# Kernel optimization log

Measured on AMD Instinct MI355X. Metric: run time of the kernel, lower is better.

The kernel has to match this reference:

```python
import jax, jax.numpy as jnp
import numpy as np

N, E = 50000, 800000
IN, HID, H, OUT = 128, 32, 4, 32
NEG_SLOPE = 0.2


def _gatv2_layer(x, edge_index, Wl, bl, Wr, br, att, bias, heads, ch, concat):
    """One GATv2Conv layer (PyG semantics: add self-loops, lin_l on source,
    lin_r on target, e = att . leaky_relu(gl_src + gr_dst), segment softmax
    over incoming edges of each target, scatter-add weighted source messages)."""
    n = x.shape[0]
    loop = jnp.arange(n)
    src = jnp.concatenate([edge_index[0], loop])
    dst = jnp.concatenate([edge_index[1], loop])

    gl = (x @ Wl + bl).reshape(n, heads, ch)   # source transform [N,H,C]
    gr = (x @ Wr + br).reshape(n, heads, ch)   # target transform [N,H,C]

    m = jax.nn.leaky_relu(gl[src] + gr[dst], NEG_SLOPE)   # [E+N,H,C]
    e = jnp.einsum('ehc,hc->eh', m, att)                   # [E+N,H]

    # numerically stable segment softmax over dst
    emax = jax.lax.stop_gradient(jax.ops.segment_max(e, dst, num_segments=n))
    ex = jnp.exp(e - emax[dst])
    denom = jax.ops.segment_sum(ex, dst, num_segments=n)
    alpha = ex / denom[dst]                                # [E+N,H]

    out = jax.ops.segment_sum(alpha[:, :, None] * gl[src], dst, num_segments=n)  # [N,H,C]
    out = out.reshape(n, heads * ch) if concat else out.mean(axis=1)
    return out + bias


def setup_inputs() -> dict:
    key = jax.random.key(0)
    ks = jax.random.split(key, 16)
    s = 0.05
    return {
        'x': jax.random.normal(ks[0], (N, IN), dtype=jnp.float32),
        'edge_index': jax.random.randint(ks[1], (2, E), 0, N, dtype=jnp.int32),
        # layer 1: IN -> HID, H heads, concat
        'Wl1': jax.random.normal(ks[2], (IN, H * HID), dtype=jnp.float32) * s,
        'bl1': jnp.zeros((H * HID,), dtype=jnp.float32),
        'Wr1': jax.random.normal(ks[3], (IN, H * HID), dtype=jnp.float32) * s,
        'br1': jnp.zeros((H * HID,), dtype=jnp.float32),
        'att1': jax.random.normal(ks[4], (H, HID), dtype=jnp.float32) * s,
        'bias1': jnp.zeros((H * HID,), dtype=jnp.float32),
        # layer 2: H*HID -> OUT, 1 head, no concat
        'Wl2': jax.random.normal(ks[5], (H * HID, OUT), dtype=jnp.float32) * s,
        'bl2': jnp.zeros((OUT,), dtype=jnp.float32),
        'Wr2': jax.random.normal(ks[6], (H * HID, OUT), dtype=jnp.float32) * s,
        'br2': jnp.zeros((OUT,), dtype=jnp.float32),
        'att2': jax.random.normal(ks[7], (1, OUT), dtype=jnp.float32) * s,
        'bias2': jnp.zeros((OUT,), dtype=jnp.float32),
    }


def reference(x, edge_index, Wl1, bl1, Wr1, br1, att1, bias1,
              Wl2, bl2, Wr2, br2, att2, bias2):
    h = jax.nn.elu(_gatv2_layer(x, edge_index, Wl1, bl1, Wr1, br1, att1, bias1, H, HID, True))
    # dropout inactive in eval mode
    return _gatv2_layer(h, edge_index, Wl2, bl2, Wr2, br2, att2, bias2, 1, OUT, False)
```

## Files before the change

### kernel.cpp

```cpp
#include <hip/hip_runtime.h>

#define NNODES 50000
#define NEDGES 800000
#define ETOT   (NNODES + NEDGES)
#define NEG 0.2f
#define BKTS 196
#define P1E 4096
#define NP1 ((ETOT + P1E - 1) / P1E)

typedef unsigned short ushort_t;
typedef unsigned int uint_t;
typedef __attribute__((ext_vector_type(8))) short short8;
typedef __attribute__((ext_vector_type(4))) float f32x4;

__device__ __forceinline__ ushort_t f2bf(float f) {
  uint_t u = __float_as_uint(f);
  u += 0x7FFFu + ((u >> 16) & 1u);
  return (ushort_t)(u >> 16);
}
__device__ __forceinline__ float bf2f(ushort_t h) {
  return __uint_as_float((uint_t)h << 16);
}

__global__ __launch_bounds__(256) void coarse_hist(const int* __restrict__ ei,
                                                   int* __restrict__ pcnt) {
  __shared__ int c[BKTS];
  for (int i = threadIdx.x; i < BKTS; i += 256) c[i] = 0;
  __syncthreads();
  int e0 = blockIdx.x * P1E;
#pragma unroll
  for (int t = 0; t < P1E / 256; ++t) {
    int i = e0 + t * 256 + (int)threadIdx.x;
    if (i < ETOT) {
      int dst = (i < NEDGES) ? ei[NEDGES + i] : (i - NEDGES);
      atomicAdd(&c[dst >> 8], 1);
    }
  }
  __syncthreads();
  for (int i = threadIdx.x; i < BKTS; i += 256)
    pcnt[i * NP1 + blockIdx.x] = c[i];
}

__global__ __launch_bounds__(64) void coarse_scan(const int* __restrict__ pcnt,
                                                  int* __restrict__ goffArr,
                                                  int* __restrict__ tot) {
  int b = blockIdx.x;
  int lane = threadIdx.x;
  int carry = 0;
  for (int k0 = 0; k0 < NP1; k0 += 64) {
    int k = k0 + lane;
    int v = (k < NP1) ? pcnt[b * NP1 + k] : 0;
    int s = v;
    for (int off = 1; off < 64; off <<= 1) {
      int u = __shfl_up(s, off);
      if (lane >= off) s += u;
    }
    if (k < NP1) goffArr[b * NP1 + k] = carry + s - v;
    carry += __shfl(s, 63);
  }
  if (lane == 0) tot[b] = carry;
}

__global__ __launch_bounds__(64) void bucket_scan(const int* __restrict__ tot,
                                                  int* __restrict__ bucketStart,
                                                  int* __restrict__ rowptr) {
  int lane = threadIdx.x;
  int carry = 0;
  for (int k0 = 0; k0 < BKTS; k0 += 64) {
    int k = k0 + lane;
    int v = (k < BKTS) ? tot[k] : 0;
    int s = v;
    for (int off = 1; off < 64; off <<= 1) {
      int u = __shfl_up(s, off);
      if (lane >= off) s += u;
    }
    if (k < BKTS) bucketStart[k] = carry + s - v;
    carry += __shfl(s, 63);
  }
  if (lane == 0) {
    bucketStart[BKTS] = carry;
    rowptr[NNODES] = ETOT;
  }
}

__global__ __launch_bounds__(256) void bin_phase1(const int* __restrict__ ei,
                                                  const int* __restrict__ bucketStart,
                                                  const int* __restrict__ goffArr,
                                                  uint_t* __restrict__ binned) {
  __shared__ int cnt[BKTS], pref[BKTS], fillL[BKTS];
  __shared__ uint_t stage[P1E];
  int e0 = blockIdx.x * P1E;
  for (int i = threadIdx.x; i < BKTS; i += 256) { cnt[i] = 0; fillL[i] = 0; }
  __syncthreads();
  uint_t mypk[P1E / 256];
  int mybkt[P1E / 256];
#pragma unroll
  for (int t = 0; t < P1E / 256; ++t) {
    int i = e0 + t * 256 + (int)threadIdx.x;
    if (i < ETOT) {
      int dst = (i < NEDGES) ? ei[NEDGES + i] : (i - NEDGES);
      int src = (i < NEDGES) ? ei[i] : dst;
      int b = dst >> 8;
      mypk[t] = (uint_t)src | ((uint_t)(dst & 255) << 16) | ((uint_t)b << 24);
      mybkt[t] = b;
      atomicAdd(&cnt[b], 1);
    } else mybkt[t] = -1;
  }
  __syncthreads();
  if (threadIdx.x == 0) {
    int r = 0;
    for (int b = 0; b < BKTS; ++b) { pref[b] = r; r += cnt[b]; }
  }
  __syncthreads();
#pragma unroll
  for (int t = 0; t < P1E / 256; ++t) {
    if (mybkt[t] >= 0) {
      int p = pref[mybkt[t]] + atomicAdd(&fillL[mybkt[t]], 1);
      stage[p] = mypk[t];
    }
  }
  __syncthreads();
  int total = (e0 + P1E <= ETOT) ? P1E : (ETOT - e0);
  for (int j = threadIdx.x; j < total; j += 256) {
    uint_t pk = stage[j];
    int b = pk >> 24;
    binned[bucketStart[b] + goffArr[b * NP1 + blockIdx.x] + (j - pref[b])] = pk;
  }
}

__global__ __launch_bounds__(256) void bin_phase2(const uint_t* __restrict__ binned,
                                                  const int* __restrict__ bucketStart,
                                                  int* __restrict__ rowptr,
                                                  int* __restrict__ csrc) {
  __shared__ int cnt[256], pref[256], fillL[256];
  __shared__ int outS[8192];
  int b = blockIdx.x;
  int base = bucketStart[b];
  int cntAll = bucketStart[b + 1] - base;
  cnt[threadIdx.x] = 0; fillL[threadIdx.x] = 0;
  __syncthreads();
  for (int j = threadIdx.x; j < cntAll; j += 256)
    atomicAdd(&cnt[(binned[base + j] >> 16) & 255], 1);
  __syncthreads();
  if (threadIdx.x == 0) {
    int r = 0;
    for (int i = 0; i < 256; ++i) { pref[i] = r; r += cnt[i]; }
  }
  __syncthreads();
  int node = b * 256 + (int)threadIdx.x;
  if (node < NNODES) rowptr[node] = base + pref[threadIdx.x];
  for (int j = threadIdx.x; j < cntAll; j += 256) {
    uint_t pk = binned[base + j];
    int d = (pk >> 16) & 255;
    int p = pref[d] + atomicAdd(&fillL[d], 1);
    outS[p] = (int)(pk & 0xFFFF);
  }
  __syncthreads();
  for (int j = threadIdx.x; j < cntAll; j += 256)
    csrc[base + j] = outS[j];
}

__global__ __launch_bounds__(256) void prep_w(const float* __restrict__ Wl1,
                                              const float* __restrict__ Wr1,
                                              ushort_t* __restrict__ WtHi,
                                              ushort_t* __restrict__ WtLo) {
  int k = blockIdx.x;
  int n = threadIdx.x;
  float w = (n < 128) ? Wl1[k * 128 + n] : Wr1[k * 128 + (n - 128)];
  ushort_t h = f2bf(w);
  WtHi[n * 128 + k] = h;
  WtLo[n * 128 + k] = f2bf(w - bf2f(h));
}

__global__ __launch_bounds__(256) void gemm1_mfma(
    const float* __restrict__ x,
    const ushort_t* __restrict__ WtHi, const ushort_t* __restrict__ WtLo,
    const float* __restrict__ bl1, const float* __restrict__ br1,
    ushort_t* __restrict__ gl1, ushort_t* __restrict__ gr1) {
  constexpr int LDA = 132;
  __shared__ __align__(16) char smem[32 * 260 * 4];
  ushort_t (*Ahi)[LDA] = (ushort_t(*)[LDA])smem;
  ushort_t (*Alo)[LDA] = (ushort_t(*)[LDA])(smem + 32 * LDA * 2);
  float (*Cs)[260] = (float(*)[260])smem;
  int m0 = blockIdx.x * 32;
  int tid = threadIdx.x;
#pragma unroll
  for (int i = 0; i < 4; ++i) {
    int it = i * 256 + tid;
    int row = it >> 5, c4 = it & 31;
    int gm = m0 + row;
    float4 v = (gm < NNODES) ? *(const float4*)&x[(size_t)gm * 128 + 4 * c4]
                             : make_float4(0.f, 0.f, 0.f, 0.f);
    ushort_t h0 = f2bf(v.x), h1 = f2bf(v.y), h2 = f2bf(v.z), h3 = f2bf(v.w);
    ushort_t l0 = f2bf(v.x - bf2f(h0)), l1 = f2bf(v.y - bf2f(h1));
    ushort_t l2 = f2bf(v.z - bf2f(h2)), l3 = f2bf(v.w - bf2f(h3));
    uint2 ph, pl;
    ph.x = (uint_t)h0 | ((uint_t)h1 << 16); ph.y = (uint_t)h2 | ((uint_t)h3 << 16);
    pl.x = (uint_t)l0 | ((uint_t)l1 << 16); pl.y = (uint_t)l2 | ((uint_t)l3 << 16);
    *(uint2*)&Ahi[row][4 * c4] = ph;
    *(uint2*)&Alo[row][4 * c4] = pl;
  }
  __syncthreads();
  int wave = tid >> 6, lane = tid & 63;
  int quad = lane >> 4, nl = lane & 15;
  int nb = wave * 64;
  f32x4 acc[2][4];
#pragma unroll
  for (int tm = 0; tm < 2; ++tm)
#pragma unroll
    for (int tn = 0; tn < 4; ++tn) acc[tm][tn] = (f32x4){0.f, 0.f, 0.f, 0.f};

#pragma unroll
  for (int kc = 0; kc < 4; ++kc) {
    int klane = kc * 32 + quad * 8;
    short8 ah[2], al[2], bh[4], bl[4];
#pragma unroll
    for (int tm = 0; tm < 2; ++tm) {
      ah[tm] = *(const short8*)&Ahi[16 * tm + nl][klane];
      al[tm] = *(const short8*)&Alo[16 * tm + nl][klane];
    }
#pragma unroll
    for (int tn = 0; tn < 4; ++tn) {
      size_t wo = (size_t)(nb + 16 * tn + nl) * 128 + klane;
      bh[tn] = *(const short8*)&WtHi[wo];
      bl[tn] = *(const short8*)&WtLo[wo];
    }
#pragma unroll
    for (int tm = 0; tm < 2; ++tm)
#pragma unroll
      for (int tn = 0; tn < 4; ++tn) {
        acc[tm][tn] = __builtin_amdgcn_mfma_f32_16x16x32_bf16(ah[tm], bh[tn], acc[tm][tn], 0, 0, 0);
        acc[tm][tn] = __builtin_amdgcn_mfma_f32_16x16x32_bf16(ah[tm], bl[tn], acc[tm][tn], 0, 0, 0);
        acc[tm][tn] = __builtin_amdgcn_mfma_f32_16x16x32_bf16(al[tm], bh[tn], acc[tm][tn], 0, 0, 0);
      }
  }
  float bb[4];
#pragma unroll
  for (int tn = 0; tn < 4; ++tn) {
    int n = nb + 16 * tn + nl;
    bb[tn] = (n < 128) ? bl1[n] : br1[n - 128];
  }
  __syncthreads();
#pragma unroll
  for (int tm = 0; tm < 2; ++tm)
#pragma unroll
    for (int tn = 0; tn < 4; ++tn)
#pragma unroll
      for (int r = 0; r < 4; ++r)
        Cs[16 * tm + 4 * quad + r][nb + 16 * tn + nl] = acc[tm][tn][r] + bb[tn];
  __syncthreads();
#pragma unroll
  for (int i = 0; i < 2; ++i) {
    int it = i * 256 + tid;
    int row = it >> 4, oc = (it & 15) * 8;
    int gm = m0 + row;
    if (gm < NNODES) {
      uint4 pk;
      pk.x = (uint_t)f2bf(Cs[row][oc + 0]) | ((uint_t)f2bf(Cs[row][oc + 1]) << 16);
      pk.y = (uint_t)f2bf(Cs[row][oc + 2]) | ((uint_t)f2bf(Cs[row][oc + 3]) << 16);
      pk.z = (uint_t)f2bf(Cs[row][oc + 4]) | ((uint_t)f2bf(Cs[row][oc + 5]) << 16);
      pk.w = (uint_t)f2bf(Cs[row][oc + 6]) | ((uint_t)f2bf(Cs[row][oc + 7]) << 16);
      *(uint4*)&gl1[(size_t)gm * 128 + oc] = pk;
    }
  }
#pragma unroll
  for (int i = 0; i < 2; ++i) {
    int it = i * 256 + tid;
    int row = it >> 4, oc = (it & 15) * 8;
    int gm = m0 + row;
    if (gm < NNODES) {
      uint4 pk;
      pk.x = (uint_t)f2bf(Cs[row][128 + oc + 0]) | ((uint_t)f2bf(Cs[row][128 + oc + 1]) << 16);
      pk.y = (uint_t)f2bf(Cs[row][128 + oc + 2]) | ((uint_t)f2bf(Cs[row][128 + oc + 3]) << 16);
      pk.z = (uint_t)f2bf(Cs[row][128 + oc + 4]) | ((uint_t)f2bf(Cs[row][128 + oc + 5]) << 16);
      pk.w = (uint_t)f2bf(Cs[row][128 + oc + 6]) | ((uint_t)f2bf(Cs[row][128 + oc + 7]) << 16);
      *(uint4*)&gr1[(size_t)gm * 128 + oc] = pk;
    }
  }
}

__global__ __launch_bounds__(128) void gemm2_tile(
    const ushort_t* __restrict__ A,
    const float* __restrict__ W1, const float* __restrict__ b1,
    const float* __restrict__ W2, const float* __restrict__ b2,
    ushort_t* __restrict__ G1, ushort_t* __restrict__ G2) {
  constexpr int K = 128, KC = 32, BM = 128, BN = 64, MCOLS = 32, NT = 128;
  constexpr int LDA = BM + 4;
  __shared__ float AsT[KC][LDA];
  __shared__ float Ws[KC][BN];
  int row0 = blockIdx.x * BM;
  int tid = threadIdx.x;
  int tx = tid % (BN / 8), ty = tid / (BN / 8);
  float acc[8][8];
#pragma unroll
  for (int i = 0; i < 8; ++i)
#pragma unroll
    for (int j = 0; j < 8; ++j) acc[i][j] = 0.f;

  for (int kc = 0; kc < K; kc += KC) {
#pragma unroll
    for (int item = tid; item < BM * (KC / 4); item += NT) {
      int r = item >> 3, f4 = item & 7;
      int grow = row0 + r;
      uint2 u = (grow < NNODES)
          ? *(const uint2*)&A[(size_t)grow * K + kc + 4 * f4]
          : make_uint2(0u, 0u);
      AsT[4 * f4 + 0][r] = __uint_as_float(u.x << 16);
      AsT[4 * f4 + 1][r] = __uint_as_float(u.x & 0xffff0000u);
      AsT[4 * f4 + 2][r] = __uint_as_float(u.y << 16);
      AsT[4 * f4 + 3][r] = __uint_as_float(u.y & 0xffff0000u);
    }
#pragma unroll
    for (int item = tid; item < KC * (BN / 4); item += NT) {
      int k = item / (BN / 4), c4 = item % (BN / 4);
      int ccat = 4 * c4;
      const float* src = (ccat < MCOLS)
          ? &W1[(size_t)(kc + k) * MCOLS + ccat]
          : &W2[(size_t)(kc + k) * MCOLS + ccat - MCOLS];
      *(float4*)&Ws[k][4 * c4] = *(const float4*)src;
    }
    __syncthreads();
#pragma unroll 8
    for (int k = 0; k < KC; ++k) {
      float4 a0 = *(const float4*)&AsT[k][4 * ty];
      float4 a1 = *(const float4*)&AsT[k][BM / 2 + 4 * ty];
      float4 w0 = *(const float4*)&Ws[k][4 * tx];
      float4 w1 = *(const float4*)&Ws[k][BN / 2 + 4 * tx];
      float av[8] = {a0.x, a0.y, a0.z, a0.w, a1.x, a1.y, a1.z, a1.w};
      float wv[8] = {w0.x, w0.y, w0.z, w0.w, w1.x, w1.y, w1.z, w1.w};
#pragma unroll
      for (int i = 0; i < 8; ++i)
#pragma unroll
        for (int j = 0; j < 8; ++j) acc[i][j] = fmaf(av[i], wv[j], acc[i][j]);
    }
    __syncthreads();
  }
#pragma unroll
  for (int i = 0; i < 8; ++i) {
    int row = row0 + (i < 4 ? 4 * ty + i : BM / 2 + 4 * ty + (i - 4));
    if (row >= NNODES) continue;
#pragma unroll
    for (int jj = 0; jj < 2; ++jj) {
      int ccat = (jj == 0 ? 4 * tx : BN / 2 + 4 * tx);
      float o0 = acc[i][4 * jj + 0], o1 = acc[i][4 * jj + 1];
      float o2 = acc[i][4 * jj + 2], o3 = acc[i][4 * jj + 3];
      if (ccat < MCOLS) {
        float4 bb = *(const float4*)&b1[ccat];
        uint2 pk;
        pk.x = (uint_t)f2bf(o0 + bb.x) | ((uint_t)f2bf(o1 + bb.y) << 16);
        pk.y = (uint_t)f2bf(o2 + bb.z) | ((uint_t)f2bf(o3 + bb.w) << 16);
        *(uint2*)&G1[(size_t)row * MCOLS + ccat] = pk;
      } else {
        int c = ccat - MCOLS;
        float4 bb = *(const float4*)&b2[c];
        uint2 pk;
        pk.x = (uint_t)f2bf(o0 + bb.x) | ((uint_t)f2bf(o1 + bb.y) << 16);
        pk.y = (uint_t)f2bf(o2 + bb.z) | ((uint_t)f2bf(o3 + bb.w) << 16);
        *(uint2*)&G2[(size_t)row * MCOLS + c] = pk;
      }
    }
  }
}

__global__ __launch_bounds__(128) void gat1_edge(const int* __restrict__ rowptr,
                          const int* __restrict__ csrc,
                          const ushort_t* __restrict__ glb,
                          const ushort_t* __restrict__ grb,
                          const float* __restrict__ att, const float* __restrict__ bias,
                          ushort_t* __restrict__ hout) {
  int node = blockIdx.x * 2 + (threadIdx.x >> 6);
  if (node >= NNODES) return;
  int lane = threadIdx.x & 63;
  int eslot = lane >> 4;
  int q = lane & 15;
  int c8 = q * 8;
  const float C6 = 0.8656170245333781f;
  const float C4 = 0.5770780163555854f;
  float4 av0 = *(const float4*)(att + c8);
  float4 av1 = *(const float4*)(att + c8 + 4);
  float4 a60, a61, a40, a41;
  a60.x = C6 * av0.x; a60.y = C6 * av0.y; a60.z = C6 * av0.z; a60.w = C6 * av0.w;
  a61.x = C6 * av1.x; a61.y = C6 * av1.y; a61.z = C6 * av1.z; a61.w = C6 * av1.w;
  a40.x = C4 * av0.x; a40.y = C4 * av0.y; a40.z = C4 * av0.z; a40.w = C4 * av0.w;
  a41.x = C4 * av1.x; a41.y = C4 * av1.y; a41.z = C4 * av1.z; a41.w = C4 * av1.w;
  uint4 ug = *(const uint4*)(grb + (size_t)node * 128 + c8);
  float4 gr0, gr1v;
  gr0.x = __uint_as_float(ug.x << 16);  gr0.y = __uint_as_float(ug.x & 0xffff0000u);
  gr0.z = __uint_as_float(ug.y << 16);  gr0.w = __uint_as_float(ug.y & 0xffff0000u);
  gr1v.x = __uint_as_float(ug.z << 16); gr1v.y = __uint_as_float(ug.z & 0xffff0000u);
  gr1v.z = __uint_as_float(ug.w << 16); gr1v.w = __uint_as_float(ug.w & 0xffff0000u);
  int start = rowptr[node], end = rowptr[node + 1];
  float denom = 0.f;
  float4 A0 = make_float4(0.f, 0.f, 0.f, 0.f);
  float4 A1 = make_float4(0.f, 0.f, 0.f, 0.f);
  const char* glc = (const char*)glb;
  uint_t coff = (uint_t)(c8 * 2);
  for (int b = start; b < end; b += 64) {
    int nb = end - b; if (nb > 64) nb = 64;
    int sidx = (lane < nb) ? csrc[b + lane] : 0;
    int s0 = __shfl(sidx, eslot);
    uint4 up = *(const uint4*)(glc + (((uint_t)s0 << 8) + coff));
    for (int j = 0; j < nb; j += 4) {
      bool pv = (j + eslot) < nb;
      int jn = j + 4 + eslot;
      int jc = (jn < nb) ? jn : 0;
      int sn = __shfl(sidx, jc);
      uint4 upn = *(const uint4*)(glc + (((uint_t)sn << 8) + coff));
      float4 g0, g1;
      g0.x = __uint_as_float(up.x << 16);
      g0.y = __uint_as_float(up.x & 0xffff0000u);
      g0.z = __uint_as_float(up.y << 16);
      g0.w = __uint_as_float(up.y & 0xffff0000u);
      g1.x = __uint_as_float(up.z << 16);
      g1.y = __uint_as_float(up.z & 0xffff0000u);
      g1.z = __uint_as_float(up.w << 16);
      g1.w = __uint_as_float(up.w & 0xffff0000u);
      float t, v;
      t = g0.x + gr0.x;  v = fmaf(a40.x, fabsf(t), a60.x * t);
      t = g0.y + gr0.y;  v = fmaf(a60.y, t, v); v = fmaf(a40.y, fabsf(t), v);
      t = g0.z + gr0.z;  v = fmaf(a60.z, t, v); v = fmaf(a40.z, fabsf(t), v);
      t = g0.w + gr0.w;  v = fmaf(a60.w, t, v); v = fmaf(a40.w, fabsf(t), v);
      t = g1.x + gr1v.x; v = fmaf(a61.x, t, v); v = fmaf(a41.x, fabsf(t), v);
      t = g1.y + gr1v.y; v = fmaf(a61.y, t, v); v = fmaf(a41.y, fabsf(t), v);
      t = g1.z + gr1v.z; v = fmaf(a61.z, t, v); v = fmaf(a41.z, fabsf(t), v);
      t = g1.w + gr1v.w; v = fmaf(a61.w, t, v); v = fmaf(a41.w, fabsf(t), v);
      v += __shfl_xor(v, 1); v += __shfl_xor(v, 2);
      float ex = pv ? exp2f(v) : 0.f;
      denom += ex;
      A0.x = fmaf(ex, g0.x, A0.x); A0.y = fmaf(ex, g0.y, A0.y);
      A0.z = fmaf(ex, g0.z, A0.z); A0.w = fmaf(ex, g0.w, A0.w);
      A1.x = fmaf(ex, g1.x, A1.x); A1.y = fmaf(ex, g1.y, A1.y);
      A1.z = fmaf(ex, g1.z, A1.z); A1.w = fmaf(ex, g1.w, A1.w);
      up = upn;
    }
  }
  denom += __shfl_xor(denom, 16); denom += __shfl_xor(denom, 32);
  A0.x += __shfl_xor(A0.x, 16); A0.x += __shfl_xor(A0.x, 32);
  A0.y += __shfl_xor(A0.y, 16); A0.y += __shfl_xor(A0.y, 32);
  A0.z += __shfl_xor(A0.z, 16); A0.z += __shfl_xor(A0.z, 32);
  A0.w += __shfl_xor(A0.w, 16); A0.w += __shfl_xor(A0.w, 32);
  A1.x += __shfl_xor(A1.x, 16); A1.x += __shfl_xor(A1.x, 32);
  A1.y += __shfl_xor(A1.y, 16); A1.y += __shfl_xor(A1.y, 32);
  A1.z += __shfl_xor(A1.z, 16); A1.z += __shfl_xor(A1.z, 32);
  A1.w += __shfl_xor(A1.w, 16); A1.w += __shfl_xor(A1.w, 32);
  float inv = __builtin_amdgcn_rcpf(denom);
  if (eslot == 0) {
    float4 bv = *(const float4*)(bias + c8);
    float o0 = A0.x * inv + bv.x, o1 = A0.y * inv + bv.y;
    float o2 = A0.z * inv + bv.z, o3 = A0.w * inv + bv.w;
    o0 = o0 > 0.f ? o0 : __expf(o0) - 1.f;
    o1 = o1 > 0.f ? o1 : __expf(o1) - 1.f;
    o2 = o2 > 0.f ? o2 : __expf(o2) - 1.f;
    o3 = o3 > 0.f ? o3 : __expf(o3) - 1.f;
    uint2 pk;
    pk.x = (uint_t)f2bf(o0) | ((uint_t)f2bf(o1) << 16);
    pk.y = (uint_t)f2bf(o2) | ((uint_t)f2bf(o3) << 16);
    *(uint2*)&hout[(size_t)node * 128 + c8] = pk;
  } else if (eslot == 1) {
    float4 bv = *(const float4*)(bias + c8 + 4);
    float o0 = A1.x * inv + bv.x, o1 = A1.y * inv + bv.y;
    float o2 = A1.z * inv + bv.z, o3 = A1.w * inv + bv.w;
    o0 = o0 > 0.f ? o0 : __expf(o0) - 1.f;
    o1 = o1 > 0.f ? o1 : __expf(o1) - 1.f;
    o2 = o2 > 0.f ? o2 : __expf(o2) - 1.f;
    o3 = o3 > 0.f ? o3 : __expf(o3) - 1.f;
    uint2 pk;
    pk.x = (uint_t)f2bf(o0) | ((uint_t)f2bf(o1) << 16);
    pk.y = (uint_t)f2bf(o2) | ((uint_t)f2bf(o3) << 16);
    *(uint2*)&hout[(size_t)node * 128 + c8 + 4] = pk;
  }
}

__global__ __launch_bounds__(128) void gat2_edge(const int* __restrict__ rowptr,
                          const int* __restrict__ csrc,
                          const ushort_t* __restrict__ gl, const ushort_t* __restrict__ gr,
                          const float* __restrict__ att, const float* __restrict__ bias,
                          float* __restrict__ out) {
  int node = blockIdx.x * 2 + (threadIdx.x >> 6);
  if (node >= NNODES) return;
  int lane = threadIdx.x & 63;
  int eslot = lane >> 3;
  int q = lane & 7;
  int c4 = q * 4;
  const float C6 = 0.8656170245333781f;
  const float C4f = 0.5770780163555854f;
  float4 avc = *(const float4*)(att + c4);
  float4 a6, a4;
  a6.x = C6 * avc.x; a6.y = C6 * avc.y; a6.z = C6 * avc.z; a6.w = C6 * avc.w;
  a4.x = C4f * avc.x; a4.y = C4f * avc.y; a4.z = C4f * avc.z; a4.w = C4f * avc.w;
  uint2 ugr = *(const uint2*)(gr + (size_t)node * 32 + c4);
  float4 grd;
  grd.x = __uint_as_float(ugr.x << 16); grd.y = __uint_as_float(ugr.x & 0xffff0000u);
  grd.z = __uint_as_float(ugr.y << 16); grd.w = __uint_as_float(ugr.y & 0xffff0000u);
  int start = rowptr[node], end = rowptr[node + 1];
  float denom = 0.f;
  float4 A = make_float4(0.f, 0.f, 0.f, 0.f);
  const char* glc = (const char*)gl;
  uint_t coff = (uint_t)(c4 * 2);
  for (int b = start; b < end; b += 64) {
    int nb = end - b; if (nb > 64) nb = 64;
    int sidx = (lane < nb) ? csrc[b + lane] : 0;
    int s0 = __shfl(sidx, eslot);
    uint2 ugl = *(const uint2*)(glc + (((uint_t)s0 << 6) + coff));
    for (int j = 0; j < nb; j += 8) {
      bool pv = (j + eslot) < nb;
      int jn = j + 8 + eslot;
      int jc = (jn < nb) ? jn : 0;
      int sn = __shfl(sidx, jc);
      uint2 ugn = *(const uint2*)(glc + (((uint_t)sn << 6) + coff));
      float4 g;
      g.x = __uint_as_float(ugl.x << 16); g.y = __uint_as_float(ugl.x & 0xffff0000u);
      g.z = __uint_as_float(ugl.y << 16); g.w = __uint_as_float(ugl.y & 0xffff0000u);
      float t, v;
      t = g.x + grd.x; v = fmaf(a4.x, fabsf(t), a6.x * t);
      t = g.y + grd.y; v = fmaf(a6.y, t, v); v = fmaf(a4.y, fabsf(t), v);
      t = g.z + grd.z; v = fmaf(a6.z, t, v); v = fmaf(a4.z, fabsf(t), v);
      t = g.w + grd.w; v = fmaf(a6.w, t, v); v = fmaf(a4.w, fabsf(t), v);
      v += __shfl_xor(v, 1); v += __shfl_xor(v, 2); v += __shfl_xor(v, 4);
      float ex = pv ? exp2f(v) : 0.f;
      denom += ex;
      A.x = fmaf(ex, g.x, A.x); A.y = fmaf(ex, g.y, A.y);
      A.z = fmaf(ex, g.z, A.z); A.w = fmaf(ex, g.w, A.w);
      ugl = ugn;
    }
  }
  denom += __shfl_xor(denom, 8); denom += __shfl_xor(denom, 16); denom += __shfl_xor(denom, 32);
  A.x += __shfl_xor(A.x, 8); A.x += __shfl_xor(A.x, 16); A.x += __shfl_xor(A.x, 32);
  A.y += __shfl_xor(A.y, 8); A.y += __shfl_xor(A.y, 16); A.y += __shfl_xor(A.y, 32);
  A.z += __shfl_xor(A.z, 8); A.z += __shfl_xor(A.z, 16); A.z += __shfl_xor(A.z, 32);
  A.w += __shfl_xor(A.w, 8); A.w += __shfl_xor(A.w, 16); A.w += __shfl_xor(A.w, 32);
  if (eslot == 0) {
    float inv = __builtin_amdgcn_rcpf(denom);
    float4 bv = *(const float4*)(bias + c4);
    float4 o;
    o.x = A.x * inv + bv.x; o.y = A.y * inv + bv.y;
    o.z = A.z * inv + bv.z; o.w = A.w * inv + bv.w;
    *(float4*)(out + (size_t)node * 32 + c4) = o;
  }
}

extern "C" void kernel_launch(void* const* d_in, const int* in_sizes, int n_in,
                              void* d_out, int out_size, void* d_ws, size_t ws_size,
                              hipStream_t stream) {
  const float* x     = (const float*)d_in[0];
  const int*   ei    = (const int*)  d_in[1];
  const float* Wl1   = (const float*)d_in[2];
  const float* bl1   = (const float*)d_in[3];
  const float* Wr1   = (const float*)d_in[4];
  const float* br1   = (const float*)d_in[5];
  const float* att1  = (const float*)d_in[6];
  const float* bias1 = (const float*)d_in[7];
  const float* Wl2   = (const float*)d_in[8];
  const float* bl2   = (const float*)d_in[9];
  const float* Wr2   = (const float*)d_in[10];
  const float* br2   = (const float*)d_in[11];
  const float* att2  = (const float*)d_in[12];
  const float* bias2 = (const float*)d_in[13];
  float* out = (float*)d_out;

  char* w = (char*)d_ws;
  auto carve = [&](size_t bytes) {
    char* p = w;
    w += (bytes + 255) & ~(size_t)255;
    return p;
  };
  ushort_t* gl1 = (ushort_t*)carve((size_t)NNODES * 128 * 2);
  ushort_t* gr1 = (ushort_t*)carve((size_t)NNODES * 128 * 2);
  ushort_t* h   = (ushort_t*)carve((size_t)NNODES * 128 * 2);
  ushort_t* gl2 = (ushort_t*)carve((size_t)NNODES * 32 * 2);
  ushort_t* gr2 = (ushort_t*)carve((size_t)NNODES * 32 * 2);
  ushort_t* WtHi = (ushort_t*)carve((size_t)256 * 128 * 2);
  ushort_t* WtLo = (ushort_t*)carve((size_t)256 * 128 * 2);
  int* pcnt    = (int*)carve((size_t)NP1 * BKTS * 4);
  int* goffArr = (int*)carve((size_t)NP1 * BKTS * 4);
  int* tot     = (int*)carve((size_t)BKTS * 4);
  int* bucketStart = (int*)carve((size_t)(BKTS + 1) * 4);
  int* rowptr = (int*)carve((size_t)(NNODES + 1) * 4);
  uint_t* binned = (uint_t*)carve((size_t)ETOT * 4);
  int* csrc = (int*)carve((size_t)ETOT * 4);

  prep_w<<<128, 256, 0, stream>>>(Wl1, Wr1, WtHi, WtLo);
  coarse_hist<<<NP1, 256, 0, stream>>>(ei, pcnt);
  coarse_scan<<<BKTS, 64, 0, stream>>>(pcnt, goffArr, tot);
  bucket_scan<<<1, 64, 0, stream>>>(tot, bucketStart, rowptr);
  bin_phase1<<<NP1, 256, 0, stream>>>(ei, bucketStart, goffArr, binned);
  bin_phase2<<<BKTS, 256, 0, stream>>>(binned, bucketStart, rowptr, csrc);

  gemm1_mfma<<<(NNODES + 31) / 32, 256, 0, stream>>>(x, WtHi, WtLo, bl1, br1, gl1, gr1);
  gat1_edge<<<(NNODES + 1) / 2, 128, 0, stream>>>(rowptr, csrc, gl1, gr1, att1, bias1, h);
  gemm2_tile<<<(NNODES + 127) / 128, 128, 0, stream>>>(h, Wl2, bl2, Wr2, br2, gl2, gr2);
  gat2_edge<<<(NNODES + 1) / 2, 128, 0, stream>>>(rowptr, csrc, gl2, gr2, att2, bias2, out);
}
```

Baseline: 261.1 us.

## Co-schedule independent CSR binning and GEMM1 blocks in shared kernel launches

Independent stages are merged into heterogeneous launches: weight prep runs alongside the coarse histogram, and the layer-1 GEMM is split in two halves that share launches with the two binning phases. This removes launch gaps and lets the small, poorly occupied binning kernels overlap with compute-heavy GEMM blocks. It also replaces the serial single-thread prefix sums with wave-level scans and precomputes edge validity predicates in the edge loops. The risk is that the shared larger LDS allocation lowers occupancy for the binning blocks, and the split point is hard-coded.

```diff
diff --git a/kernel.cpp b/kernel.cpp
--- a/kernel.cpp
+++ b/kernel.cpp
@@ -7,6 +7,9 @@
 #define BKTS 196
 #define P1E 4096
 #define NP1 ((ETOT + P1E - 1) / P1E)
+#define GEMM1_NB ((NNODES + 31) / 32)
+#define GEMM1_H1 782
+#define GEMM1_H2 (GEMM1_NB - GEMM1_H1)
 
 typedef unsigned short ushort_t;
 typedef unsigned int uint_t;
@@ -22,168 +25,141 @@
   return __uint_as_float((uint_t)h << 16);
 }
 
-__global__ __launch_bounds__(256) void coarse_hist(const int* __restrict__ ei,
-                                                   int* __restrict__ pcnt) {
-  __shared__ int c[BKTS];
-  for (int i = threadIdx.x; i < BKTS; i += 256) c[i] = 0;
-  __syncthreads();
-  int e0 = blockIdx.x * P1E;
+
+__device__ __forceinline__ void coarse_hist_body(int bid, int tid,
+    const int* __restrict__ ei, int* __restrict__ pcnt, int* c ) {
+  for (int i = tid; i < BKTS; i += 256) c[i] = 0;
+  __syncthreads();
+  int e0 = bid * P1E;
 #pragma unroll
   for (int t = 0; t < P1E / 256; ++t) {
-    int i = e0 + t * 256 + (int)threadIdx.x;
+    int i = e0 + t * 256 + tid;
     if (i < ETOT) {
       int dst = (i < NEDGES) ? ei[NEDGES + i] : (i - NEDGES);
       atomicAdd(&c[dst >> 8], 1);
     }
   }
   __syncthreads();
-  for (int i = threadIdx.x; i < BKTS; i += 256)
-    pcnt[i * NP1 + blockIdx.x] = c[i];
-}
-
-__global__ __launch_bounds__(64) void coarse_scan(const int* __restrict__ pcnt,
-                                                  int* __restrict__ goffArr,
-                                                  int* __restrict__ tot) {
-  int b = blockIdx.x;
-  int lane = threadIdx.x;
-  int carry = 0;
-  for (int k0 = 0; k0 < NP1; k0 += 64) {
-    int k = k0 + lane;
-    int v = (k < NP1) ? pcnt[b * NP1 + k] : 0;
-    int s = v;
-    for (int off = 1; off < 64; off <<= 1) {
-      int u = __shfl_up(s, off);
-      if (lane >= off) s += u;
-    }
-    if (k < NP1) goffArr[b * NP1 + k] = carry + s - v;
-    carry += __shfl(s, 63);
-  }
-  if (lane == 0) tot[b] = carry;
-}
-
-__global__ __launch_bounds__(64) void bucket_scan(const int* __restrict__ tot,
-                                                  int* __restrict__ bucketStart,
-                                                  int* __restrict__ rowptr) {
-  int lane = threadIdx.x;
-  int carry = 0;
-  for (int k0 = 0; k0 < BKTS; k0 += 64) {
-    int k = k0 + lane;
-    int v = (k < BKTS) ? tot[k] : 0;
-    int s = v;
-    for (int off = 1; off < 64; off <<= 1) {
-      int u = __shfl_up(s, off);
-      if (lane >= off) s += u;
-    }
-    if (k < BKTS) bucketStart[k] = carry + s - v;
-    carry += __shfl(s, 63);
-  }
-  if (lane == 0) {
-    bucketStart[BKTS] = carry;
-    rowptr[NNODES] = ETOT;
-  }
-}
-
-__global__ __launch_bounds__(256) void bin_phase1(const int* __restrict__ ei,
-                                                  const int* __restrict__ bucketStart,
-                                                  const int* __restrict__ goffArr,
-                                                  uint_t* __restrict__ binned) {
-  __shared__ int cnt[BKTS], pref[BKTS], fillL[BKTS];
-  __shared__ uint_t stage[P1E];
-  int e0 = blockIdx.x * P1E;
-  for (int i = threadIdx.x; i < BKTS; i += 256) { cnt[i] = 0; fillL[i] = 0; }
+  for (int i = tid; i < BKTS; i += 256)
+    pcnt[i * NP1 + bid] = c[i];
+}
+
+__device__ __forceinline__ void prep_w_body(int k, int n,
+    const float* __restrict__ Wl1, const float* __restrict__ Wr1,
+    ushort_t* __restrict__ WtHi, ushort_t* __restrict__ WtLo) {
+  float w = (n < 128) ? Wl1[k * 128 + n] : Wr1[k * 128 + (n - 128)];
+  ushort_t h = f2bf(w);
+  WtHi[n * 128 + k] = h;
+  WtLo[n * 128 + k] = f2bf(w - bf2f(h));
+}
+
+__device__ __forceinline__ void bin1_body(int bid, int tid,
+    const int* __restrict__ ei, const int* __restrict__ bucketStart,
+    const int* __restrict__ goffArr, uint_t* __restrict__ binned, char* smemc) {
+  int* cnt   = (int*)smemc;
+  int* pref  = cnt + BKTS;
+  int* fillL = pref + BKTS;
+  uint_t* stage = (uint_t*)(fillL + BKTS);
+  int e0 = bid * P1E;
+  for (int i = tid; i < BKTS; i += 256) { cnt[i] = 0; fillL[i] = 0; }
   __syncthreads();
   uint_t mypk[P1E / 256];
-  int mybkt[P1E / 256];
 #pragma unroll
   for (int t = 0; t < P1E / 256; ++t) {
-    int i = e0 + t * 256 + (int)threadIdx.x;
+    int i = e0 + t * 256 + tid;
     if (i < ETOT) {
       int dst = (i < NEDGES) ? ei[NEDGES + i] : (i - NEDGES);
       int src = (i < NEDGES) ? ei[i] : dst;
       int b = dst >> 8;
       mypk[t] = (uint_t)src | ((uint_t)(dst & 255) << 16) | ((uint_t)b << 24);
-      mybkt[t] = b;
       atomicAdd(&cnt[b], 1);
-    } else mybkt[t] = -1;
-  }
-  __syncthreads();
-  if (threadIdx.x == 0) {
-    int r = 0;
-    for (int b = 0; b < BKTS; ++b) { pref[b] = r; r += cnt[b]; }
+    } else mypk[t] = 0xFFFFFFFFu;
+  }
+  __syncthreads();
+  if (tid < 64) {
+    int carry = 0;
+    for (int k0 = 0; k0 < BKTS; k0 += 64) {
+      int k = k0 + tid;
+      int v = (k < BKTS) ? cnt[k] : 0;
+      int s = v;
+      for (int off = 1; off < 64; off <<= 1) {
+        int u = __shfl_up(s, off);
+        if (tid >= off) s += u;
+      }
+      if (k < BKTS) pref[k] = carry + s - v;
+      carry += __shfl(s, 63);
+    }
   }
   __syncthreads();
 #pragma unroll
   for (int t = 0; t < P1E / 256; ++t) {
-    if (mybkt[t] >= 0) {
-      int p = pref[mybkt[t]] + atomicAdd(&fillL[mybkt[t]], 1);
-      stage[p] = mypk[t];
+    uint_t pk = mypk[t];
+    int b = pk >> 24;
+    if (b < BKTS) {
+      int p = pref[b] + atomicAdd(&fillL[b], 1);
+      stage[p] = pk;
     }
   }
   __syncthreads();
   int total = (e0 + P1E <= ETOT) ? P1E : (ETOT - e0);
-  for (int j = threadIdx.x; j < total; j += 256) {
+  for (int j = tid; j < total; j += 256) {
     uint_t pk = stage[j];
     int b = pk >> 24;
-    binned[bucketStart[b] + goffArr[b * NP1 + blockIdx.x] + (j - pref[b])] = pk;
-  }
-}
-
-__global__ __launch_bounds__(256) void bin_phase2(const uint_t* __restrict__ binned,
-                                                  const int* __restrict__ bucketStart,
-                                                  int* __restrict__ rowptr,
-                                                  int* __restrict__ csrc) {
-  __shared__ int cnt[256], pref[256], fillL[256];
-  __shared__ int outS[8192];
-  int b = blockIdx.x;
+    binned[bucketStart[b] + goffArr[b * NP1 + bid] + (j - pref[b])] = pk;
+  }
+}
+
+__device__ __forceinline__ void bin2_body(int b, int tid,
+    const uint_t* __restrict__ binned, const int* __restrict__ bucketStart,
+    int* __restrict__ rowptr, int* __restrict__ csrc, char* smemc) {
+  int* cnt   = (int*)smemc;
+  int* pref  = cnt + 256;
+  int* fillL = pref + 256;
+  int* outS  = fillL + 256;
   int base = bucketStart[b];
   int cntAll = bucketStart[b + 1] - base;
-  cnt[threadIdx.x] = 0; fillL[threadIdx.x] = 0;
-  __syncthreads();
-  for (int j = threadIdx.x; j < cntAll; j += 256)
+  cnt[tid] = 0; fillL[tid] = 0;
+  __syncthreads();
+  for (int j = tid; j < cntAll; j += 256)
     atomicAdd(&cnt[(binned[base + j] >> 16) & 255], 1);
   __syncthreads();
-  if (threadIdx.x == 0) {
-    int r = 0;
-    for (int i = 0; i < 256; ++i) { pref[i] = r; r += cnt[i]; }
-  }
-  __syncthreads();
-  int node = b * 256 + (int)threadIdx.x;
-  if (node < NNODES) rowptr[node] = base + pref[threadIdx.x];
-  for (int j = threadIdx.x; j < cntAll; j += 256) {
+  if (tid < 64) {
+    int carry = 0;
+    for (int k0 = 0; k0 < 256; k0 += 64) {
+      int k = k0 + tid;
+      int v = cnt[k];
+      int s = v;
+      for (int off = 1; off < 64; off <<= 1) {
+        int u = __shfl_up(s, off);
+        if (tid >= off) s += u;
+      }
+      pref[k] = carry + s - v;
+      carry += __shfl(s, 63);
+    }
+  }
+  __syncthreads();
+  int node = b * 256 + tid;
+  if (node < NNODES) rowptr[node] = base + pref[tid];
+  for (int j = tid; j < cntAll; j += 256) {
     uint_t pk = binned[base + j];
     int d = (pk >> 16) & 255;
     int p = pref[d] + atomicAdd(&fillL[d], 1);
     outS[p] = (int)(pk & 0xFFFF);
   }
   __syncthreads();
-  for (int j = threadIdx.x; j < cntAll; j += 256)
+  for (int j = tid; j < cntAll; j += 256)
     csrc[base + j] = outS[j];
 }
 
-__global__ __launch_bounds__(256) void prep_w(const float* __restrict__ Wl1,
-                                              const float* __restrict__ Wr1,
-                                              ushort_t* __restrict__ WtHi,
-                                              ushort_t* __restrict__ WtLo) {
-  int k = blockIdx.x;
-  int n = threadIdx.x;
-  float w = (n < 128) ? Wl1[k * 128 + n] : Wr1[k * 128 + (n - 128)];
-  ushort_t h = f2bf(w);
-  WtHi[n * 128 + k] = h;
-  WtLo[n * 128 + k] = f2bf(w - bf2f(h));
-}
-
-__global__ __launch_bounds__(256) void gemm1_mfma(
+__device__ __forceinline__ void gemm1_body(int m0, int tid,
     const float* __restrict__ x,
     const ushort_t* __restrict__ WtHi, const ushort_t* __restrict__ WtLo,
     const float* __restrict__ bl1, const float* __restrict__ br1,
-    ushort_t* __restrict__ gl1, ushort_t* __restrict__ gr1) {
+    ushort_t* __restrict__ gl1, ushort_t* __restrict__ gr1, char* smem) {
   constexpr int LDA = 132;
-  __shared__ __align__(16) char smem[32 * 260 * 4];
   ushort_t (*Ahi)[LDA] = (ushort_t(*)[LDA])smem;
   ushort_t (*Alo)[LDA] = (ushort_t(*)[LDA])(smem + 32 * LDA * 2);
   float (*Cs)[260] = (float(*)[260])smem;
-  int m0 = blockIdx.x * 32;
-  int tid = threadIdx.x;
 #pragma unroll
   for (int i = 0; i < 4; ++i) {
     int it = i * 256 + tid;
@@ -277,6 +253,85 @@
       *(uint4*)&gr1[(size_t)gm * 128 + oc] = pk;
     }
   }
+}
+
+
+__global__ __launch_bounds__(256) void fusedA(const int* __restrict__ ei,
+    int* __restrict__ pcnt,
+    const float* __restrict__ Wl1, const float* __restrict__ Wr1,
+    ushort_t* __restrict__ WtHi, ushort_t* __restrict__ WtLo) {
+  __shared__ int c[BKTS];
+  int bid = blockIdx.x, tid = threadIdx.x;
+  if (bid < NP1) coarse_hist_body(bid, tid, ei, pcnt, c);
+  else           prep_w_body(bid - NP1, tid, Wl1, Wr1, WtHi, WtLo);
+}
+
+__global__ __launch_bounds__(64) void coarse_scan(const int* __restrict__ pcnt,
+                                                  int* __restrict__ goffArr,
+                                                  int* __restrict__ tot) {
+  int b = blockIdx.x;
+  int lane = threadIdx.x;
+  int carry = 0;
+  for (int k0 = 0; k0 < NP1; k0 += 64) {
+    int k = k0 + lane;
+    int v = (k < NP1) ? pcnt[b * NP1 + k] : 0;
+    int s = v;
+    for (int off = 1; off < 64; off <<= 1) {
+      int u = __shfl_up(s, off);
+      if (lane >= off) s += u;
+    }
+    if (k < NP1) goffArr[b * NP1 + k] = carry + s - v;
+    carry += __shfl(s, 63);
+  }
+  if (lane == 0) tot[b] = carry;
+}
+
+__global__ __launch_bounds__(64) void bucket_scan(const int* __restrict__ tot,
+                                                  int* __restrict__ bucketStart,
+                                                  int* __restrict__ rowptr) {
+  int lane = threadIdx.x;
+  int carry = 0;
+  for (int k0 = 0; k0 < BKTS; k0 += 64) {
+    int k = k0 + lane;
+    int v = (k < BKTS) ? tot[k] : 0;
+    int s = v;
+    for (int off = 1; off < 64; off <<= 1) {
+      int u = __shfl_up(s, off);
+      if (lane >= off) s += u;
+    }
+    if (k < BKTS) bucketStart[k] = carry + s - v;
+    carry += __shfl(s, 63);
+  }
+  if (lane == 0) {
+    bucketStart[BKTS] = carry;
+    rowptr[NNODES] = ETOT;
+  }
+}
+
+__global__ __launch_bounds__(256) void fusedB(const int* __restrict__ ei,
+    const int* __restrict__ bucketStart, const int* __restrict__ goffArr,
+    uint_t* __restrict__ binned,
+    const float* __restrict__ x,
+    const ushort_t* __restrict__ WtHi, const ushort_t* __restrict__ WtLo,
+    const float* __restrict__ bl1, const float* __restrict__ br1,
+    ushort_t* __restrict__ gl1, ushort_t* __restrict__ gr1) {
+  __shared__ __align__(16) char smem[32 * 260 * 4];
+  int bid = blockIdx.x, tid = threadIdx.x;
+  if (bid < NP1) bin1_body(bid, tid, ei, bucketStart, goffArr, binned, smem);
+  else gemm1_body((bid - NP1) * 32, tid, x, WtHi, WtLo, bl1, br1, gl1, gr1, smem);
+}
+
+__global__ __launch_bounds__(256) void fusedC(const uint_t* __restrict__ binned,
+    const int* __restrict__ bucketStart, int* __restrict__ rowptr,
+    int* __restrict__ csrc,
+    const float* __restrict__ x,
+    const ushort_t* __restrict__ WtHi, const ushort_t* __restrict__ WtLo,
+    const float* __restrict__ bl1, const float* __restrict__ br1,
+    ushort_t* __restrict__ gl1, ushort_t* __restrict__ gr1) {
+  __shared__ __align__(16) char smem[32 * 260 * 4];
+  int bid = blockIdx.x, tid = threadIdx.x;
+  if (bid < BKTS) bin2_body(bid, tid, binned, bucketStart, rowptr, csrc, smem);
+  else gemm1_body((GEMM1_H1 + bid - BKTS) * 32, tid, x, WtHi, WtLo, bl1, br1, gl1, gr1, smem);
 }
 
 __global__ __launch_bounds__(128) void gemm2_tile(
@@ -398,13 +453,13 @@
   for (int b = start; b < end; b += 64) {
     int nb = end - b; if (nb > 64) nb = 64;
     int sidx = (lane < nb) ? csrc[b + lane] : 0;
+    bool pv = eslot < nb;
     int s0 = __shfl(sidx, eslot);
     uint4 up = *(const uint4*)(glc + (((uint_t)s0 << 8) + coff));
     for (int j = 0; j < nb; j += 4) {
-      bool pv = (j + eslot) < nb;
       int jn = j + 4 + eslot;
-      int jc = (jn < nb) ? jn : 0;
-      int sn = __shfl(sidx, jc);
+      bool pvn = jn < nb;
+      int sn = __shfl(sidx, pvn ? jn : 0);
       uint4 upn = *(const uint4*)(glc + (((uint_t)sn << 8) + coff));
       float4 g0, g1;
       g0.x = __uint_as_float(up.x << 16);
@@ -431,7 +486,7 @@
       A0.z = fmaf(ex, g0.z, A0.z); A0.w = fmaf(ex, g0.w, A0.w);
       A1.x = fmaf(ex, g1.x, A1.x); A1.y = fmaf(ex, g1.y, A1.y);
       A1.z = fmaf(ex, g1.z, A1.z); A1.w = fmaf(ex, g1.w, A1.w);
-      up = upn;
+      up = upn; pv = pvn;
     }
   }
   denom += __shfl_xor(denom, 16); denom += __shfl_xor(denom, 32);
@@ -500,13 +555,13 @@
   for (int b = start; b < end; b += 64) {
     int nb = end - b; if (nb > 64) nb = 64;
     int sidx = (lane < nb) ? csrc[b + lane] : 0;
+    bool pv = eslot < nb;
     int s0 = __shfl(sidx, eslot);
     uint2 ugl = *(const uint2*)(glc + (((uint_t)s0 << 6) + coff));
     for (int j = 0; j < nb; j += 8) {
-      bool pv = (j + eslot) < nb;
       int jn = j + 8 + eslot;
-      int jc = (jn < nb) ? jn : 0;
-      int sn = __shfl(sidx, jc);
+      bool pvn = jn < nb;
+      int sn = __shfl(sidx, pvn ? jn : 0);
       uint2 ugn = *(const uint2*)(glc + (((uint_t)sn << 6) + coff));
       float4 g;
       g.x = __uint_as_float(ugl.x << 16); g.y = __uint_as_float(ugl.x & 0xffff0000u);
@@ -521,7 +576,7 @@
       denom += ex;
       A.x = fmaf(ex, g.x, A.x); A.y = fmaf(ex, g.y, A.y);
       A.z = fmaf(ex, g.z, A.z); A.w = fmaf(ex, g.w, A.w);
-      ugl = ugn;
+      ugl = ugn; pv = pvn;
     }
   }
   denom += __shfl_xor(denom, 8); denom += __shfl_xor(denom, 16); denom += __shfl_xor(denom, 32);
@@ -579,14 +634,13 @@
   uint_t* binned = (uint_t*)carve((size_t)ETOT * 4);
   int* csrc = (int*)carve((size_t)ETOT * 4);
 
-  prep_w<<<128, 256, 0, stream>>>(Wl1, Wr1, WtHi, WtLo);
-  coarse_hist<<<NP1, 256, 0, stream>>>(ei, pcnt);
+  fusedA<<<NP1 + 128, 256, 0, stream>>>(ei, pcnt, Wl1, Wr1, WtHi, WtLo);
   coarse_scan<<<BKTS, 64, 0, stream>>>(pcnt, goffArr, tot);
   bucket_scan<<<1, 64, 0, stream>>>(tot, bucketStart, rowptr);
-  bin_phase1<<<NP1, 256, 0, stream>>>(ei, bucketStart, goffArr, binned);
-  bin_phase2<<<BKTS, 256, 0, stream>>>(binned, bucketStart, rowptr, csrc);
-
-  gemm1_mfma<<<(NNODES + 31) / 32, 256, 0, stream>>>(x, WtHi, WtLo, bl1, br1, gl1, gr1);
+  fusedB<<<NP1 + GEMM1_H1, 256, 0, stream>>>(ei, bucketStart, goffArr, binned,
+                                             x, WtHi, WtLo, bl1, br1, gl1, gr1);
+  fusedC<<<BKTS + GEMM1_H2, 256, 0, stream>>>(binned, bucketStart, rowptr, csrc,
+                                              x, WtHi, WtLo, bl1, br1, gl1, gr1);
   gat1_edge<<<(NNODES + 1) / 2, 128, 0, stream>>>(rowptr, csrc, gl1, gr1, att1, bias1, h);
   gemm2_tile<<<(NNODES + 127) / 128, 128, 0, stream>>>(h, Wl2, bl2, Wr2, br2, gl2, gr2);
   gat2_edge<<<(NNODES + 1) / 2, 128, 0, stream>>>(rowptr, csrc, gl2, gr2, att2, bias2, out);
```

New measurement: 247.0 us. 5.4% less time.
